# Kernel tuning notes

Hardware: AMD Instinct MI355X
Metric: run time of the kernel (lower is better)

Reference implementation:

```python
import jax, jax.numpy as jnp
import numpy as np
from jax import lax

SIGMA = 5
RADIUS = int(4 * SIGMA + 0.5)  # 20 -> kernel size 41, pad_size = 41//2 = 20 = RADIUS
D_AP = 2.27
D_DV = 2.27


def _gauss_d1_kernel():
    # gaussian_kernel1d(sigma, order=1, radius): q(x) = -x/sigma^2, kernel = q(x)*phi(x)
    x = np.arange(-RADIUS, RADIUS + 1).astype(np.float64)
    phi = np.exp(-0.5 / SIGMA ** 2 * x ** 2)
    phi = phi / phi.sum()
    return ((-x / SIGMA ** 2) * phi).astype(np.float32)

_KERNEL = jnp.asarray(_gauss_d1_kernel())


def _conv1d_valid(x, k):
    # x: [N, L], k: [K] -> [N, L-K+1]; cross-correlation, same as torch F.conv1d
    return lax.conv_general_dilated(x[:, None, :], k[None, None, :], (1,), 'VALID')[:, 0, :]


def diffY(x):
    # circular padding along H, derivative / dDV
    c, h, w = x.shape
    xp = jnp.pad(x, ((0, 0), (RADIUS, RADIUS), (0, 0)), mode='wrap')
    xp = jnp.transpose(xp, (0, 2, 1)).reshape(c * w, h + 2 * RADIUS)
    out = _conv1d_valid(xp, _KERNEL).reshape(c, w, h)
    return jnp.transpose(out, (0, 2, 1)) / D_DV


def diffX(x):
    # reflect padding along W, derivative / dAP
    c, h, w = x.shape
    xp = jnp.pad(x, ((0, 0), (0, 0), (RADIUS, RADIUS)), mode='reflect')
    out = _conv1d_valid(xp.reshape(c * h, w + 2 * RADIUS), _KERNEL).reshape(c, h, w)
    return out / D_AP


def setup_inputs() -> dict:
    key = jax.random.key(0)
    k1, k2, k3, k4, k5 = jax.random.split(key, 5)
    H, W = 1024, 2048
    return {
        'y': jax.random.normal(k1, (5, H, W), dtype=jnp.float32),
        'v': jax.random.normal(k2, (2, H, W), dtype=jnp.float32),
        'gamma_ds': jax.random.normal(k3, (H, W), dtype=jnp.float32),
        'cad_coefs': jax.random.uniform(k4, (3,), dtype=jnp.float32),
        'myo_coefs': jax.random.uniform(k5, (5,), dtype=jnp.float32),
    }


def reference(y, v, gamma_ds, cad_coefs, myo_coefs):
    H, W = y.shape[-2:]
    m4 = y[:4]                                  # [4,H,W] myosin components
    c1 = y[4:]                                  # [1,H,W] cadherin

    d1_m = jnp.stack([diffY(m4), diffX(m4)], axis=-1).reshape(2, 2, H, W, 2)
    m = m4.reshape(2, 2, H, W)
    d1_c = jnp.stack([diffY(c1), diffX(c1)], axis=-1).reshape(H, W, 2)
    c = c1[0]

    d1_v = jnp.stack([diffY(v), diffX(v)], axis=-1)   # [2,H,W,2]: d1_v[i,y,x,j] = d_j v_i
    gv = jnp.einsum('iyxj->ijyx', d1_v)
    gvT = jnp.einsum('jyxi->ijyx', d1_v)
    O = -0.5 * (gv - gvT)                       # vorticity
    E = 0.5 * (gv + gvT)                        # strain rate

    eye = jnp.eye(2, dtype=y.dtype)[:, :, None, None]
    trm_yx = jnp.einsum('kkyx->yx', m)
    deviatoric = m - 0.5 * trm_yx[None, None] * eye

    m_norm = jnp.sqrt(jnp.sum(m * m, axis=(0, 1), keepdims=True))            # [1,1,H,W]
    m_0 = jnp.mean(m_norm, axis=(2, 3), keepdims=True)                       # [1,1,1,1]
    dev_mag = jnp.sqrt(jnp.sum(deviatoric * deviatoric, axis=(0, 1), keepdims=True))
    devE = jnp.einsum('klyx,klyx->yx', deviatoric, E)[None, None]

    E_active = E - jnp.sign(devE) * devE * deviatoric / dev_mag ** 2
    E_active = 0.5 * E_active * dev_mag / m_0
    E_passive = E - E_active

    mE = (jnp.einsum('ikyx,kjyx->ijyx', m, E_passive)
          + jnp.einsum('ikyx,kjyx->ijyx', E_passive, m))

    cad = jax.nn.relu(cad_coefs)
    myo = jax.nn.relu(myo_coefs)

    cdot = (-jnp.einsum('iyx,yxi->yx', v, d1_c)
            - cad[0] * c
            + cad[1] * c * jnp.einsum('iyxi->yx', d1_v)
            + cad[2] * gamma_ds)

    trm = trm_yx[None, None]
    gamma_dv = jnp.array([[1.0, 0.0], [0.0, 0.0]], dtype=y.dtype)[:, :, None, None]

    mdot = (-jnp.einsum('kyx,ijyxk->ijyx', v, d1_m)
            - jnp.einsum('ikyx,kjyx->ijyx', O, m)
            + jnp.einsum('ikyx,kjyx->ijyx', m, O)
            - myo[0] * m
            + myo[1] * mE
            - myo[2] * c[None, None] * mE
            + myo[3] * trm * gamma_dv
            + myo[4] * trm * m)

    return jnp.concatenate([mdot.reshape(4, H, W), cdot[None]], axis=0)
```

## Files before the change

kernel.cpp:

```cpp
#include <hip/hip_runtime.h>
#include <math.h>

#define RAD 20
#define KLEN 41
#define NH 1024
#define NW 2048
#define NHW (NH * NW)

struct KW { float w[KLEN]; };
constexpr double cexp_neg(double u) {
  double term = 1.0, sum = 1.0;
  for (int k = 1; k < 30; ++k) { term *= (-u) / (double)k; sum += term; }
  return sum;
}
constexpr KW make_kw() {
  KW r{};
  double ph[KLEN] = {};
  double s = 0.0;
  for (int i = 0; i < KLEN; ++i) {
    double d = (double)(i - RAD);
    double e = cexp_neg(d * d / 800.0);
    e = e * e; e = e * e; e = e * e; e = e * e;
    ph[i] = e; s += e;
  }
  for (int i = 0; i < KLEN; ++i) {
    double d = (double)(i - RAD);
    r.w[i] = (float)((-d / 25.0) * (ph[i] / s) / 2.27);
  }
  return r;
}
static constexpr KW KWC = make_kw();

template <int K>
__device__ __forceinline__ void tap(float s, float& r0, float& r1, float& r2,
                                    float& r3, float& r4, float& r5, float& r6,
                                    float& r7) {
  if constexpr (K - 0 >= 0 && K - 0 <= 40) r0 = fmaf(s, KWC.w[K - 0], r0);
  if constexpr (K - 1 >= 0 && K - 1 <= 40) r1 = fmaf(s, KWC.w[K - 1], r1);
  if constexpr (K - 2 >= 0 && K - 2 <= 40) r2 = fmaf(s, KWC.w[K - 2], r2);
  if constexpr (K - 3 >= 0 && K - 3 <= 40) r3 = fmaf(s, KWC.w[K - 3], r3);
  if constexpr (K - 4 >= 0 && K - 4 <= 40) r4 = fmaf(s, KWC.w[K - 4], r4);
  if constexpr (K - 5 >= 0 && K - 5 <= 40) r5 = fmaf(s, KWC.w[K - 5], r5);
  if constexpr (K - 6 >= 0 && K - 6 <= 40) r6 = fmaf(s, KWC.w[K - 6], r6);
  if constexpr (K - 7 >= 0 && K - 7 <= 40) r7 = fmaf(s, KWC.w[K - 7], r7);
}

#define R8 r0, r1, r2, r3, r4, r5, r6, r7

#define TW 64
#define TH 32
#define TILE_CH ((TH + 2 * RAD) * TW)

__device__ __forceinline__ void conv_col(const float* __restrict__ t, int base,
                                         int lane, float& r0, float& r1,
                                         float& r2, float& r3, float& r4,
                                         float& r5, float& r6, float& r7) {
#define CCHUNK(c)                                      \
  {                                                    \
    float s0 = t[(base + 4 * (c) + 0) * TW + lane];    \
    float s1 = t[(base + 4 * (c) + 1) * TW + lane];    \
    float s2 = t[(base + 4 * (c) + 2) * TW + lane];    \
    float s3 = t[(base + 4 * (c) + 3) * TW + lane];    \
    tap<4 * (c) + 0>(s0, R8);                          \
    tap<4 * (c) + 1>(s1, R8);                          \
    tap<4 * (c) + 2>(s2, R8);                          \
    tap<4 * (c) + 3>(s3, R8);                          \
  }
  CCHUNK(0) CCHUNK(1) CCHUNK(2) CCHUNK(3) CCHUNK(4) CCHUNK(5)
  CCHUNK(6) CCHUNK(7) CCHUNK(8) CCHUNK(9) CCHUNK(10) CCHUNK(11)
#undef CCHUNK
}

__global__ __launch_bounds__(256) void k_dx(const float* __restrict__ y,
                                            const float* __restrict__ v,
                                            float* __restrict__ ws,
                                            double* __restrict__ acc) {
  __shared__ float row[2120];
  __shared__ double rsm[4];
  const int t = threadIdx.x;
  const int r = blockIdx.x;
  const int ch = blockIdx.y;
  const float* src = (ch < 5) ? (y + (size_t)ch * NHW) : (v + (size_t)(ch - 5) * NHW);
  const float* rp = src + (size_t)r * NW;

#define SWZ(i) ((i) + ((i) >> 6))
#define ST(i, val) { const int ii_ = (i); row[SWZ(ii_)] = (val); }

  const float4* rp4 = (const float4*)rp;
  float4 b0 = rp4[t];
  float4 b1 = rp4[t + 256];

  float4 a1x, a1y, a2x, a2y, a3x, a3y;
  if (ch == 0) {
    const float4* p1 = (const float4*)(y + (size_t)NHW + (size_t)r * NW);
    const float4* p2 = (const float4*)(y + 2 * (size_t)NHW + (size_t)r * NW);
    const float4* p3 = (const float4*)(y + 3 * (size_t)NHW + (size_t)r * NW);
    a1x = p1[t]; a1y = p1[t + 256];
    a2x = p2[t]; a2y = p2[t + 256];
    a3x = p3[t]; a3y = p3[t + 256];
  }

  ST(RAD + 4 * t + 0, b0.x)
  ST(RAD + 4 * t + 1, b0.y)
  ST(RAD + 4 * t + 2, b0.z)
  ST(RAD + 4 * t + 3, b0.w)
  ST(RAD + 4 * (t + 256) + 0, b1.x)
  ST(RAD + 4 * (t + 256) + 1, b1.y)
  ST(RAD + 4 * (t + 256) + 2, b1.z)
  ST(RAD + 4 * (t + 256) + 3, b1.w)
  if (t < RAD) {
    ST(t, rp[RAD - t])
    ST(NW + RAD + t, rp[NW - 2 - t])
  }
  __syncthreads();

  const int xb = 8 * t;
  float r0 = 0.f, r1 = 0.f, r2 = 0.f, r3 = 0.f;
  float r4 = 0.f, r5 = 0.f, r6 = 0.f, r7 = 0.f;
#define RD(k) { const int x_ = xb + (k); float s_ = row[SWZ(x_)]; tap<(k)>(s_, R8); }
  RD(0)  RD(1)  RD(2)  RD(3)  RD(4)  RD(5)  RD(6)  RD(7)
  RD(8)  RD(9)  RD(10) RD(11) RD(12) RD(13) RD(14) RD(15)
  RD(16) RD(17) RD(18) RD(19) RD(20) RD(21) RD(22) RD(23)
  RD(24) RD(25) RD(26) RD(27) RD(28) RD(29) RD(30) RD(31)
  RD(32) RD(33) RD(34) RD(35) RD(36) RD(37) RD(38) RD(39)
  RD(40) RD(41) RD(42) RD(43) RD(44) RD(45) RD(46) RD(47)
#undef RD

  float4 o0, o1;
  o0.x = r0; o0.y = r1; o0.z = r2; o0.w = r3;
  o1.x = r4; o1.y = r5; o1.z = r6; o1.w = r7;
  float4* dst = (float4*)(ws + (size_t)(7 + ch) * NHW + (size_t)r * NW + xb);
  dst[0] = o0;
  dst[1] = o1;

  if (ch == 0) {
    double local =
        (double)sqrtf(b0.x * b0.x + a1x.x * a1x.x + a2x.x * a2x.x + a3x.x * a3x.x) +
        (double)sqrtf(b0.y * b0.y + a1x.y * a1x.y + a2x.y * a2x.y + a3x.y * a3x.y) +
        (double)sqrtf(b0.z * b0.z + a1x.z * a1x.z + a2x.z * a2x.z + a3x.z * a3x.z) +
        (double)sqrtf(b0.w * b0.w + a1x.w * a1x.w + a2x.w * a2x.w + a3x.w * a3x.w) +
        (double)sqrtf(b1.x * b1.x + a1y.x * a1y.x + a2y.x * a2y.x + a3y.x * a3y.x) +
        (double)sqrtf(b1.y * b1.y + a1y.y * a1y.y + a2y.y * a2y.y + a3y.y * a3y.y) +
        (double)sqrtf(b1.z * b1.z + a1y.z * a1y.z + a2y.z * a2y.z + a3y.z * a3y.z) +
        (double)sqrtf(b1.w * b1.w + a1y.w * a1y.w + a2y.w * a2y.w + a3y.w * a3y.w);
#pragma unroll
    for (int off = 32; off > 0; off >>= 1) local += __shfl_down(local, off, 64);
    const int lane = t & 63;
    const int wid = t >> 6;
    if (lane == 0) rsm[wid] = local;
    __syncthreads();
    if (t == 0) atomicAdd(acc, rsm[0] + rsm[1] + rsm[2] + rsm[3]);
  }
}

__global__ __launch_bounds__(256, 4) void k_dyf(
    const float* __restrict__ y, const float* __restrict__ v,
    const float* __restrict__ gds, const float* __restrict__ cadc,
    const float* __restrict__ myoc, const float* __restrict__ ws,
    const double* __restrict__ acc, float* __restrict__ out) {
  __shared__ float tile[2 * TILE_CH];
  const int lane = threadIdx.x & 63;
  const int wid = threadIdx.x >> 6;
  const int x0 = blockIdx.x * TW;
  const int yb = blockIdx.y * TH;
  const int base = wid * 8;

  const float m0 = (float)(acc[0] / (double)NHW);
  const float cad0 = fmaxf(cadc[0], 0.f);
  const float cad1 = fmaxf(cadc[1], 0.f);
  const float cad2 = fmaxf(cadc[2], 0.f);
  const float my0 = fmaxf(myoc[0], 0.f);
  const float my1 = fmaxf(myoc[1], 0.f);
  const float my2 = fmaxf(myoc[2], 0.f);
  const float my3 = fmaxf(myoc[3], 0.f);
  const float my4 = fmaxf(myoc[4], 0.f);

#define SGLD(sp, k) \
  (sp)[(size_t)(((yb - RAD + wid + 4 * (k)) + NH) & (NH - 1)) * NW + x0 + lane]

  float u0, u1, u2, u3, u4, u5, u6, u7, u8;
  float u9, u10, u11, u12, u13, u14, u15, u16, u17;

#define LOADCH(srcp)                                                   \
  {                                                                    \
    const float* sp_ = (srcp);                                         \
    u0 = SGLD(sp_, 0); u1 = SGLD(sp_, 1); u2 = SGLD(sp_, 2);           \
    u3 = SGLD(sp_, 3); u4 = SGLD(sp_, 4); u5 = SGLD(sp_, 5);           \
    u6 = SGLD(sp_, 6); u7 = SGLD(sp_, 7); u8 = SGLD(sp_, 8);           \
    u9 = SGLD(sp_, 9); u10 = SGLD(sp_, 10); u11 = SGLD(sp_, 11);       \
    u12 = SGLD(sp_, 12); u13 = SGLD(sp_, 13); u14 = SGLD(sp_, 14);     \
    u15 = SGLD(sp_, 15); u16 = SGLD(sp_, 16); u17 = SGLD(sp_, 17);     \
  }
#define WRITECH(g)                                                        \
  {                                                                       \
    float* tb_ = &tile[(g) * TILE_CH];                                    \
    tb_[(wid + 0) * TW + lane] = u0;   tb_[(wid + 4) * TW + lane] = u1;   \
    tb_[(wid + 8) * TW + lane] = u2;   tb_[(wid + 12) * TW + lane] = u3;  \
    tb_[(wid + 16) * TW + lane] = u4;  tb_[(wid + 20) * TW + lane] = u5;  \
    tb_[(wid + 24) * TW + lane] = u6;  tb_[(wid + 28) * TW + lane] = u7;  \
    tb_[(wid + 32) * TW + lane] = u8;  tb_[(wid + 36) * TW + lane] = u9;  \
    tb_[(wid + 40) * TW + lane] = u10; tb_[(wid + 44) * TW + lane] = u11; \
    tb_[(wid + 48) * TW + lane] = u12; tb_[(wid + 52) * TW + lane] = u13; \
    tb_[(wid + 56) * TW + lane] = u14; tb_[(wid + 60) * TW + lane] = u15; \
    tb_[(wid + 64) * TW + lane] = u16; tb_[(wid + 68) * TW + lane] = u17; \
  }
#define DECL8(P)                                                       \
  float P##0 = 0.f, P##1 = 0.f, P##2 = 0.f, P##3 = 0.f, P##4 = 0.f,    \
        P##5 = 0.f, P##6 = 0.f, P##7 = 0.f;
#define CALLCONV(g, P)                                                  \
  conv_col(&tile[(g) * TILE_CH], base, lane, P##0, P##1, P##2, P##3,    \
           P##4, P##5, P##6, P##7);

  DECL8(ym00) DECL8(ym01) DECL8(ym10) DECL8(ym11)
  DECL8(yc) DECL8(yv0) DECL8(yv1)

  LOADCH(y)
  WRITECH(0)
  __syncthreads();
  LOADCH(y + (size_t)NHW)
  CALLCONV(0, ym00)
  WRITECH(1)
  __syncthreads();
  LOADCH(y + 2 * (size_t)NHW)
  CALLCONV(1, ym01)
  WRITECH(0)
  __syncthreads();
  LOADCH(y + 3 * (size_t)NHW)
  CALLCONV(0, ym10)
  WRITECH(1)
  __syncthreads();
  LOADCH(y + 4 * (size_t)NHW)
  CALLCONV(1, ym11)
  WRITECH(0)
  __syncthreads();
  LOADCH(v)
  CALLCONV(0, yc)
  WRITECH(1)
  __syncthreads();
  LOADCH(v + (size_t)NHW)
  CALLCONV(1, yv0)
  WRITECH(0)
  __syncthreads();
  CALLCONV(0, yv1)

#define POINT(q)                                                              \
  {                                                                           \
    const size_t idx = (size_t)(yb + base + (q)) * NW + x0 + lane;            \
    const float m00 = y[idx];                                                 \
    const float m01 = y[idx + (size_t)NHW];                                   \
    const float m10 = y[idx + 2 * (size_t)NHW];                               \
    const float m11 = y[idx + 3 * (size_t)NHW];                               \
    const float c = y[idx + 4 * (size_t)NHW];                                 \
    const float v0 = v[idx];                                                  \
    const float v1 = v[idx + (size_t)NHW];                                    \
    const float g = gds[idx];                                                 \
    const float dY_m00 = ym00##q, dY_m01 = ym01##q;                           \
    const float dY_m10 = ym10##q, dY_m11 = ym11##q;                           \
    const float dY_c = yc##q, dY_v0 = yv0##q, dY_v1 = yv1##q;                 \
    const float dX_m00 = ws[idx + 7 * (size_t)NHW];                           \
    const float dX_m01 = ws[idx + 8 * (size_t)NHW];                           \
    const float dX_m10 = ws[idx + 9 * (size_t)NHW];                           \
    const float dX_m11 = ws[idx + 10 * (size_t)NHW];                          \
    const float dX_c = ws[idx + 11 * (size_t)NHW];                            \
    const float dX_v0 = ws[idx + 12 * (size_t)NHW];                           \
    const float dX_v1 = ws[idx + 13 * (size_t)NHW];                           \
    const float gv00 = dY_v0, gv01 = dX_v0, gv10 = dY_v1, gv11 = dX_v1;       \
    const float ww = -0.5f * (gv01 - gv10);                                   \
    const float E00 = gv00, E11 = gv11;                                       \
    const float E01 = 0.5f * (gv01 + gv10);                                   \
    const float E10 = E01;                                                    \
    const float trm = m00 + m11;                                              \
    const float dev00 = m00 - 0.5f * trm;                                     \
    const float dev01 = m01;                                                  \
    const float dev10 = m10;                                                  \
    const float dev11 = m11 - 0.5f * trm;                                     \
    const float dmag_sq =                                                     \
        dev00 * dev00 + dev01 * dev01 + dev10 * dev10 + dev11 * dev11;        \
    const float dm = sqrtf(dmag_sq);                                          \
    const float dm2 = dm * dm;                                                \
    const float devE = dev00 * E00 + dev01 * E01 + dev10 * E10 + dev11 * E11; \
    const float sg = (devE > 0.f) ? 1.f : ((devE < 0.f) ? -1.f : 0.f);        \
    const float coef = sg * devE / dm2;                                       \
    const float sc = 0.5f * dm / m0;                                          \
    const float Ea00 = (E00 - coef * dev00) * sc;                             \
    const float Ea01 = (E01 - coef * dev01) * sc;                             \
    const float Ea10 = (E10 - coef * dev10) * sc;                             \
    const float Ea11 = (E11 - coef * dev11) * sc;                             \
    const float Ep00 = E00 - Ea00;                                            \
    const float Ep01 = E01 - Ea01;                                            \
    const float Ep10 = E10 - Ea10;                                            \
    const float Ep11 = E11 - Ea11;                                            \
    const float mE00 = (m00 * Ep00 + m01 * Ep10) + (Ep00 * m00 + Ep01 * m10); \
    const float mE01 = (m00 * Ep01 + m01 * Ep11) + (Ep00 * m01 + Ep01 * m11); \
    const float mE10 = (m10 * Ep00 + m11 * Ep10) + (Ep10 * m00 + Ep11 * m10); \
    const float mE11 = (m10 * Ep01 + m11 * Ep11) + (Ep10 * m01 + Ep11 * m11); \
    const float divv = gv00 + gv11;                                           \
    const float cdot =                                                        \
        -(v0 * dY_c + v1 * dX_c) - cad0 * c + cad1 * c * divv + cad2 * g;     \
    const float md00 = -(v0 * dY_m00 + v1 * dX_m00) - ww * m10 - ww * m01 -   \
                       my0 * m00 + my1 * mE00 - my2 * c * mE00 + my3 * trm +  \
                       my4 * trm * m00;                                       \
    const float md01 = -(v0 * dY_m01 + v1 * dX_m01) - ww * m11 + ww * m00 -   \
                       my0 * m01 + my1 * mE01 - my2 * c * mE01 +              \
                       my4 * trm * m01;                                       \
    const float md10 = -(v0 * dY_m10 + v1 * dX_m10) + ww * m00 - ww * m11 -   \
                       my0 * m10 + my1 * mE10 - my2 * c * mE10 +              \
                       my4 * trm * m10;                                       \
    const float md11 = -(v0 * dY_m11 + v1 * dX_m11) + ww * m01 + ww * m10 -   \
                       my0 * m11 + my1 * mE11 - my2 * c * mE11 +              \
                       my4 * trm * m11;                                       \
    out[idx] = md00;                                                          \
    out[idx + (size_t)NHW] = md01;                                            \
    out[idx + 2 * (size_t)NHW] = md10;                                        \
    out[idx + 3 * (size_t)NHW] = md11;                                        \
    out[idx + 4 * (size_t)NHW] = cdot;                                        \
  }

  POINT(0) POINT(1) POINT(2) POINT(3)
  POINT(4) POINT(5) POINT(6) POINT(7)
#undef POINT
}

extern "C" void kernel_launch(void* const* d_in, const int* in_sizes, int n_in,
                              void* d_out, int out_size, void* d_ws, size_t ws_size,
                              hipStream_t stream) {
  (void)in_sizes; (void)n_in; (void)out_size; (void)ws_size;
  const float* y = (const float*)d_in[0];
  const float* v = (const float*)d_in[1];
  const float* gds = (const float*)d_in[2];
  const float* cadc = (const float*)d_in[3];
  const float* myoc = (const float*)d_in[4];
  float* out = (float*)d_out;

  double* acc = (double*)d_ws;
  float* planes = (float*)((char*)d_ws + 512);

  hipMemsetAsync(acc, 0, sizeof(double), stream);
  k_dx<<<dim3(NH, 7), dim3(256), 0, stream>>>(y, v, planes, acc);
  k_dyf<<<dim3(NW / TW, NH / TH), dim3(256), 0, stream>>>(y, v, gds, cadc, myoc,
                                                          planes, acc, out);
}
```

Baseline: 174.8 us.

## Load x-derivative windows directly into registers and double k_dyf tile height

k_dx no longer stages each row in shared memory. Each thread now loads its 48-wide input window straight from global memory into registers, using vector loads in the interior and reflected scalar loads at the edges. This removes the LDS staging and the barrier, but neighbouring threads now re-read overlapping data from global memory or cache. k_dyf grows its tile height from 32 to 64 rows with 512 threads, which cuts the halo overhead per output row from 40/32 to 40/64 at the cost of more shared memory per block and possibly lower occupancy.

```diff
diff --git a/kernel.cpp b/kernel.cpp
--- a/kernel.cpp
+++ b/kernel.cpp
@@ -48,7 +48,7 @@
 #define R8 r0, r1, r2, r3, r4, r5, r6, r7
 
 #define TW 64
-#define TH 32
+#define TH 64
 #define TILE_CH ((TH + 2 * RAD) * TW)
 
 __device__ __forceinline__ void conv_col(const float* __restrict__ t, int base,
@@ -71,60 +71,78 @@
 #undef CCHUNK
 }
 
-__global__ __launch_bounds__(256) void k_dx(const float* __restrict__ y,
-                                            const float* __restrict__ v,
-                                            float* __restrict__ ws,
-                                            double* __restrict__ acc) {
-  __shared__ float row[2120];
+__device__ __forceinline__ int reflx(int x) {
+  int xr = x < 0 ? -x : x;
+  return xr > NW - 1 ? 2 * NW - 2 - xr : xr;
+}
+
+__global__ __launch_bounds__(256, 4) void k_dx(const float* __restrict__ y,
+                                               const float* __restrict__ v,
+                                               float* __restrict__ ws,
+                                               double* __restrict__ acc) {
   __shared__ double rsm[4];
   const int t = threadIdx.x;
+  const int lane = t & 63;
+  const int wid = t >> 6;
   const int r = blockIdx.x;
   const int ch = blockIdx.y;
   const float* src = (ch < 5) ? (y + (size_t)ch * NHW) : (v + (size_t)(ch - 5) * NHW);
   const float* rp = src + (size_t)r * NW;
 
-#define SWZ(i) ((i) + ((i) >> 6))
-#define ST(i, val) { const int ii_ = (i); row[SWZ(ii_)] = (val); }
-
-  const float4* rp4 = (const float4*)rp;
-  float4 b0 = rp4[t];
-  float4 b1 = rp4[t + 256];
-
-  float4 a1x, a1y, a2x, a2y, a3x, a3y;
-  if (ch == 0) {
-    const float4* p1 = (const float4*)(y + (size_t)NHW + (size_t)r * NW);
-    const float4* p2 = (const float4*)(y + 2 * (size_t)NHW + (size_t)r * NW);
-    const float4* p3 = (const float4*)(y + 3 * (size_t)NHW + (size_t)r * NW);
-    a1x = p1[t]; a1y = p1[t + 256];
-    a2x = p2[t]; a2y = p2[t + 256];
-    a3x = p3[t]; a3y = p3[t + 256];
-  }
-
-  ST(RAD + 4 * t + 0, b0.x)
-  ST(RAD + 4 * t + 1, b0.y)
-  ST(RAD + 4 * t + 2, b0.z)
-  ST(RAD + 4 * t + 3, b0.w)
-  ST(RAD + 4 * (t + 256) + 0, b1.x)
-  ST(RAD + 4 * (t + 256) + 1, b1.y)
-  ST(RAD + 4 * (t + 256) + 2, b1.z)
-  ST(RAD + 4 * (t + 256) + 3, b1.w)
-  if (t < RAD) {
-    ST(t, rp[RAD - t])
-    ST(NW + RAD + t, rp[NW - 2 - t])
-  }
-  __syncthreads();
-
   const int xb = 8 * t;
+  const int xs = xb - RAD;
+
+  float w0, w1, w2, w3, w4, w5, w6, w7, w8, w9, w10, w11;
+  float w12, w13, w14, w15, w16, w17, w18, w19, w20, w21, w22, w23;
+  float w24, w25, w26, w27, w28, w29, w30, w31, w32, w33, w34, w35;
+  float w36, w37, w38, w39, w40, w41, w42, w43, w44, w45, w46, w47;
+
+  if (t >= 3 && t <= 252) {
+    const float4* p = (const float4*)(rp + xs);
+    float4 f0 = p[0], f1 = p[1], f2 = p[2], f3 = p[3];
+    float4 f4 = p[4], f5 = p[5], f6 = p[6], f7 = p[7];
+    float4 f8 = p[8], f9 = p[9], f10 = p[10], f11 = p[11];
+    w0 = f0.x; w1 = f0.y; w2 = f0.z; w3 = f0.w;
+    w4 = f1.x; w5 = f1.y; w6 = f1.z; w7 = f1.w;
+    w8 = f2.x; w9 = f2.y; w10 = f2.z; w11 = f2.w;
+    w12 = f3.x; w13 = f3.y; w14 = f3.z; w15 = f3.w;
+    w16 = f4.x; w17 = f4.y; w18 = f4.z; w19 = f4.w;
+    w20 = f5.x; w21 = f5.y; w22 = f5.z; w23 = f5.w;
+    w24 = f6.x; w25 = f6.y; w26 = f6.z; w27 = f6.w;
+    w28 = f7.x; w29 = f7.y; w30 = f7.z; w31 = f7.w;
+    w32 = f8.x; w33 = f8.y; w34 = f8.z; w35 = f8.w;
+    w36 = f9.x; w37 = f9.y; w38 = f9.z; w39 = f9.w;
+    w40 = f10.x; w41 = f10.y; w42 = f10.z; w43 = f10.w;
+    w44 = f11.x; w45 = f11.y; w46 = f11.z; w47 = f11.w;
+  } else {
+    w0 = rp[reflx(xs + 0)]; w1 = rp[reflx(xs + 1)]; w2 = rp[reflx(xs + 2)];
+    w3 = rp[reflx(xs + 3)]; w4 = rp[reflx(xs + 4)]; w5 = rp[reflx(xs + 5)];
+    w6 = rp[reflx(xs + 6)]; w7 = rp[reflx(xs + 7)]; w8 = rp[reflx(xs + 8)];
+    w9 = rp[reflx(xs + 9)]; w10 = rp[reflx(xs + 10)]; w11 = rp[reflx(xs + 11)];
+    w12 = rp[reflx(xs + 12)]; w13 = rp[reflx(xs + 13)]; w14 = rp[reflx(xs + 14)];
+    w15 = rp[reflx(xs + 15)]; w16 = rp[reflx(xs + 16)]; w17 = rp[reflx(xs + 17)];
+    w18 = rp[reflx(xs + 18)]; w19 = rp[reflx(xs + 19)]; w20 = rp[reflx(xs + 20)];
+    w21 = rp[reflx(xs + 21)]; w22 = rp[reflx(xs + 22)]; w23 = rp[reflx(xs + 23)];
+    w24 = rp[reflx(xs + 24)]; w25 = rp[reflx(xs + 25)]; w26 = rp[reflx(xs + 26)];
+    w27 = rp[reflx(xs + 27)]; w28 = rp[reflx(xs + 28)]; w29 = rp[reflx(xs + 29)];
+    w30 = rp[reflx(xs + 30)]; w31 = rp[reflx(xs + 31)]; w32 = rp[reflx(xs + 32)];
+    w33 = rp[reflx(xs + 33)]; w34 = rp[reflx(xs + 34)]; w35 = rp[reflx(xs + 35)];
+    w36 = rp[reflx(xs + 36)]; w37 = rp[reflx(xs + 37)]; w38 = rp[reflx(xs + 38)];
+    w39 = rp[reflx(xs + 39)]; w40 = rp[reflx(xs + 40)]; w41 = rp[reflx(xs + 41)];
+    w42 = rp[reflx(xs + 42)]; w43 = rp[reflx(xs + 43)]; w44 = rp[reflx(xs + 44)];
+    w45 = rp[reflx(xs + 45)]; w46 = rp[reflx(xs + 46)]; w47 = rp[reflx(xs + 47)];
+  }
+
   float r0 = 0.f, r1 = 0.f, r2 = 0.f, r3 = 0.f;
   float r4 = 0.f, r5 = 0.f, r6 = 0.f, r7 = 0.f;
-#define RD(k) { const int x_ = xb + (k); float s_ = row[SWZ(x_)]; tap<(k)>(s_, R8); }
-  RD(0)  RD(1)  RD(2)  RD(3)  RD(4)  RD(5)  RD(6)  RD(7)
-  RD(8)  RD(9)  RD(10) RD(11) RD(12) RD(13) RD(14) RD(15)
-  RD(16) RD(17) RD(18) RD(19) RD(20) RD(21) RD(22) RD(23)
-  RD(24) RD(25) RD(26) RD(27) RD(28) RD(29) RD(30) RD(31)
-  RD(32) RD(33) RD(34) RD(35) RD(36) RD(37) RD(38) RD(39)
-  RD(40) RD(41) RD(42) RD(43) RD(44) RD(45) RD(46) RD(47)
-#undef RD
+#define TAPW(k) tap<k>(w##k, R8);
+  TAPW(0)  TAPW(1)  TAPW(2)  TAPW(3)  TAPW(4)  TAPW(5)  TAPW(6)  TAPW(7)
+  TAPW(8)  TAPW(9)  TAPW(10) TAPW(11) TAPW(12) TAPW(13) TAPW(14) TAPW(15)
+  TAPW(16) TAPW(17) TAPW(18) TAPW(19) TAPW(20) TAPW(21) TAPW(22) TAPW(23)
+  TAPW(24) TAPW(25) TAPW(26) TAPW(27) TAPW(28) TAPW(29) TAPW(30) TAPW(31)
+  TAPW(32) TAPW(33) TAPW(34) TAPW(35) TAPW(36) TAPW(37) TAPW(38) TAPW(39)
+  TAPW(40) TAPW(41) TAPW(42) TAPW(43) TAPW(44) TAPW(45) TAPW(46) TAPW(47)
+#undef TAPW
 
   float4 o0, o1;
   o0.x = r0; o0.y = r1; o0.z = r2; o0.w = r3;
@@ -134,26 +152,31 @@
   dst[1] = o1;
 
   if (ch == 0) {
+    const size_t ro = (size_t)r * NW + xb;
+    float4 p1a = *(const float4*)(y + (size_t)NHW + ro);
+    float4 p1b = *(const float4*)(y + (size_t)NHW + ro + 4);
+    float4 p2a = *(const float4*)(y + 2 * (size_t)NHW + ro);
+    float4 p2b = *(const float4*)(y + 2 * (size_t)NHW + ro + 4);
+    float4 p3a = *(const float4*)(y + 3 * (size_t)NHW + ro);
+    float4 p3b = *(const float4*)(y + 3 * (size_t)NHW + ro + 4);
     double local =
-        (double)sqrtf(b0.x * b0.x + a1x.x * a1x.x + a2x.x * a2x.x + a3x.x * a3x.x) +
-        (double)sqrtf(b0.y * b0.y + a1x.y * a1x.y + a2x.y * a2x.y + a3x.y * a3x.y) +
-        (double)sqrtf(b0.z * b0.z + a1x.z * a1x.z + a2x.z * a2x.z + a3x.z * a3x.z) +
-        (double)sqrtf(b0.w * b0.w + a1x.w * a1x.w + a2x.w * a2x.w + a3x.w * a3x.w) +
-        (double)sqrtf(b1.x * b1.x + a1y.x * a1y.x + a2y.x * a2y.x + a3y.x * a3y.x) +
-        (double)sqrtf(b1.y * b1.y + a1y.y * a1y.y + a2y.y * a2y.y + a3y.y * a3y.y) +
-        (double)sqrtf(b1.z * b1.z + a1y.z * a1y.z + a2y.z * a2y.z + a3y.z * a3y.z) +
-        (double)sqrtf(b1.w * b1.w + a1y.w * a1y.w + a2y.w * a2y.w + a3y.w * a3y.w);
+        (double)sqrtf(w20 * w20 + p1a.x * p1a.x + p2a.x * p2a.x + p3a.x * p3a.x) +
+        (double)sqrtf(w21 * w21 + p1a.y * p1a.y + p2a.y * p2a.y + p3a.y * p3a.y) +
+        (double)sqrtf(w22 * w22 + p1a.z * p1a.z + p2a.z * p2a.z + p3a.z * p3a.z) +
+        (double)sqrtf(w23 * w23 + p1a.w * p1a.w + p2a.w * p2a.w + p3a.w * p3a.w) +
+        (double)sqrtf(w24 * w24 + p1b.x * p1b.x + p2b.x * p2b.x + p3b.x * p3b.x) +
+        (double)sqrtf(w25 * w25 + p1b.y * p1b.y + p2b.y * p2b.y + p3b.y * p3b.y) +
+        (double)sqrtf(w26 * w26 + p1b.z * p1b.z + p2b.z * p2b.z + p3b.z * p3b.z) +
+        (double)sqrtf(w27 * w27 + p1b.w * p1b.w + p2b.w * p2b.w + p3b.w * p3b.w);
 #pragma unroll
     for (int off = 32; off > 0; off >>= 1) local += __shfl_down(local, off, 64);
-    const int lane = t & 63;
-    const int wid = t >> 6;
     if (lane == 0) rsm[wid] = local;
     __syncthreads();
     if (t == 0) atomicAdd(acc, rsm[0] + rsm[1] + rsm[2] + rsm[3]);
   }
 }
 
-__global__ __launch_bounds__(256, 4) void k_dyf(
+__global__ __launch_bounds__(512, 4) void k_dyf(
     const float* __restrict__ y, const float* __restrict__ v,
     const float* __restrict__ gds, const float* __restrict__ cadc,
     const float* __restrict__ myoc, const float* __restrict__ ws,
@@ -176,10 +199,10 @@
   const float my4 = fmaxf(myoc[4], 0.f);
 
 #define SGLD(sp, k) \
-  (sp)[(size_t)(((yb - RAD + wid + 4 * (k)) + NH) & (NH - 1)) * NW + x0 + lane]
-
-  float u0, u1, u2, u3, u4, u5, u6, u7, u8;
-  float u9, u10, u11, u12, u13, u14, u15, u16, u17;
+  (sp)[(size_t)(((yb - RAD + wid + 8 * (k)) + NH) & (NH - 1)) * NW + x0 + lane]
+
+  float u0, u1, u2, u3, u4, u5, u6;
+  float u7, u8, u9, u10, u11, u12;
 
 #define LOADCH(srcp)                                                   \
   {                                                                    \
@@ -188,21 +211,18 @@
     u3 = SGLD(sp_, 3); u4 = SGLD(sp_, 4); u5 = SGLD(sp_, 5);           \
     u6 = SGLD(sp_, 6); u7 = SGLD(sp_, 7); u8 = SGLD(sp_, 8);           \
     u9 = SGLD(sp_, 9); u10 = SGLD(sp_, 10); u11 = SGLD(sp_, 11);       \
-    u12 = SGLD(sp_, 12); u13 = SGLD(sp_, 13); u14 = SGLD(sp_, 14);     \
-    u15 = SGLD(sp_, 15); u16 = SGLD(sp_, 16); u17 = SGLD(sp_, 17);     \
+    u12 = SGLD(sp_, 12);                                               \
   }
 #define WRITECH(g)                                                        \
   {                                                                       \
     float* tb_ = &tile[(g) * TILE_CH];                                    \
-    tb_[(wid + 0) * TW + lane] = u0;   tb_[(wid + 4) * TW + lane] = u1;   \
-    tb_[(wid + 8) * TW + lane] = u2;   tb_[(wid + 12) * TW + lane] = u3;  \
-    tb_[(wid + 16) * TW + lane] = u4;  tb_[(wid + 20) * TW + lane] = u5;  \
-    tb_[(wid + 24) * TW + lane] = u6;  tb_[(wid + 28) * TW + lane] = u7;  \
-    tb_[(wid + 32) * TW + lane] = u8;  tb_[(wid + 36) * TW + lane] = u9;  \
-    tb_[(wid + 40) * TW + lane] = u10; tb_[(wid + 44) * TW + lane] = u11; \
-    tb_[(wid + 48) * TW + lane] = u12; tb_[(wid + 52) * TW + lane] = u13; \
-    tb_[(wid + 56) * TW + lane] = u14; tb_[(wid + 60) * TW + lane] = u15; \
-    tb_[(wid + 64) * TW + lane] = u16; tb_[(wid + 68) * TW + lane] = u17; \
+    tb_[(wid + 0) * TW + lane] = u0;   tb_[(wid + 8) * TW + lane] = u1;   \
+    tb_[(wid + 16) * TW + lane] = u2;  tb_[(wid + 24) * TW + lane] = u3;  \
+    tb_[(wid + 32) * TW + lane] = u4;  tb_[(wid + 40) * TW + lane] = u5;  \
+    tb_[(wid + 48) * TW + lane] = u6;  tb_[(wid + 56) * TW + lane] = u7;  \
+    tb_[(wid + 64) * TW + lane] = u8;  tb_[(wid + 72) * TW + lane] = u9;  \
+    tb_[(wid + 80) * TW + lane] = u10; tb_[(wid + 88) * TW + lane] = u11; \
+    tb_[(wid + 96) * TW + lane] = u12;                                    \
   }
 #define DECL8(P)                                                       \
   float P##0 = 0.f, P##1 = 0.f, P##2 = 0.f, P##3 = 0.f, P##4 = 0.f,    \
@@ -337,6 +357,6 @@
 
   hipMemsetAsync(acc, 0, sizeof(double), stream);
   k_dx<<<dim3(NH, 7), dim3(256), 0, stream>>>(y, v, planes, acc);
-  k_dyf<<<dim3(NW / TW, NH / TH), dim3(256), 0, stream>>>(y, v, gds, cadc, myoc,
+  k_dyf<<<dim3(NW / TW, NH / TH), dim3(512), 0, stream>>>(y, v, gds, cadc, myoc,
                                                           planes, acc, out);
 }
```

After: 283.5 us. 1.62x slower.
